# Performance work log

Measured on AMD Instinct MI355X. Metric: run time of the kernel, lower is better.

Reference implementation:

```python
import jax, jax.numpy as jnp
import numpy as np

IGNORE_INDEX = -100  # torch default; targets here are all valid but mask is honored
REDUCTION = "mean"

B, D, V = 4096, 2048, 32000


def setup_inputs() -> dict:
    key = jax.random.key(0)
    k1, k2, k3 = jax.random.split(key, 3)
    x = jax.random.normal(k1, (B, D), dtype=jnp.float32)
    # LM-head weight, scaled like typical init
    L = jax.random.normal(k2, (V, D), dtype=jnp.float32) * (1.0 / np.sqrt(D))
    target = jax.random.randint(k3, (B,), 0, V, dtype=jnp.int64)
    class_weight = jnp.ones((V,), dtype=jnp.float32)  # unnormalized per-class weight
    return {"x": x, "L": L, "target": target, "class_weight": class_weight}


def reference(x, L, target, class_weight):
    """Fused linear + weighted cross-entropy (reduction='mean', ignore_index=-100).

    Equivalent math to MyLinearCrossEntropyFunction: the torch code chunks over
    batches/classes/features with an online softmax solely to avoid materializing
    logits; the unchunked math is a single GEMM + stable log-softmax CE.
    """
    # logits: [B, V]
    logits = jnp.einsum("bd,vd->bv", x, L)
    logZ = jax.nn.logsumexp(logits, axis=1)                      # [B]
    valid = target != IGNORE_INDEX                               # [B] bool
    t_safe = jnp.where(valid, target, 0)
    gathered = jnp.take_along_axis(logits, t_safe[:, None], axis=1)[:, 0]  # [B]
    # effective per-sample weight: class weight of target, zeroed where ignored
    wt = jnp.where(valid, class_weight[t_safe], jnp.zeros((), logits.dtype))  # [B]
    per_sample = wt * (logZ - gathered)
    total = per_sample.sum()
    if REDUCTION == "mean":
        return total / wt.sum()
    return total
```

## Files before the change

### kernel.cpp

```cpp
#include <hip/hip_runtime.h>

#define B_ 4096
#define D_ 2048
#define V_ 32000

#define BM 128
#define BN 128
#define BKB 128
#define NCHUNK (V_ / 64)

typedef __attribute__((ext_vector_type(8))) int   int8v;
typedef __attribute__((ext_vector_type(4))) int   int4v;
typedef __attribute__((ext_vector_type(4))) float f32x4;

#define SCALE_A 127
#define SCALE_B 121

__device__ __forceinline__ void load_lds16(const void* g, void* l) {
    __builtin_amdgcn_global_load_lds(
        (const __attribute__((address_space(1))) void*)g,
        (__attribute__((address_space(3))) void*)l,
        16, 0, 0);
}

__global__ void cast_f32_to_fp8(const float* __restrict__ x,
                                const float* __restrict__ L,
                                unsigned int* __restrict__ xq,
                                unsigned int* __restrict__ Lq) {
    const int n4x = (B_ * D_) / 4;
    const int n4l = (V_ * D_) / 4;
    int i = blockIdx.x * blockDim.x + threadIdx.x;
    const float* in; unsigned int* out; float ps; int j;
    if (i < n4x) { in = x; out = xq; ps = 1.0f;  j = i; }
    else         { j = i - n4x; if (j >= n4l) return; in = L; out = Lq; ps = 64.0f; }
    float4 v = ((const float4*)in)[j];
    int w = __builtin_amdgcn_cvt_pk_fp8_f32(v.x * ps, v.y * ps, 0, false);
    w     = __builtin_amdgcn_cvt_pk_fp8_f32(v.z * ps, v.w * ps, w, true);
    out[j] = (unsigned)w;
}

__global__ __launch_bounds__(256)
void gemm_ce_partials(const unsigned char* __restrict__ xq,
                      const unsigned char* __restrict__ Lq,
                      const int* __restrict__ targ,
                      float2* __restrict__ partials,
                      float* __restrict__ gathered) {
    __shared__ __align__(16) unsigned char As[BM * BKB];
    __shared__ __align__(16) unsigned char Bs[BN * BKB];

    const int tid    = threadIdx.x;
    const int lane   = tid & 63;
    const int wid    = tid >> 6;
    const int wave_m = wid >> 1;
    const int wave_n = wid & 1;
    const int quad   = lane >> 4;
    const int l16    = lane & 15;
    const int swz    = l16 & 7;

    const int m0 = blockIdx.x * BM;
    const int n0 = blockIdx.y * BN;

    f32x4 acc[4][4];
#pragma unroll
    for (int i = 0; i < 4; ++i)
#pragma unroll
        for (int j = 0; j < 4; ++j)
            acc[i][j] = (f32x4){0.f, 0.f, 0.f, 0.f};

    const int p0 = ((quad ^ swz) << 4);
    const int p1 = p0 ^ 64;

    for (int kt = 0; kt < D_ / BKB; ++kt) {
        const int k0 = kt * BKB;
#pragma unroll
        for (int p = 0; p < 4; ++p) {
            int flat = p * 256 + tid;
            int row  = flat >> 3;
            int pc   = flat & 7;
            int c    = pc ^ (row & 7);
            load_lds16(xq + (size_t)(m0 + row) * D_ + k0 + c * 16, &As[flat * 16]);
            load_lds16(Lq + (size_t)(n0 + row) * D_ + k0 + c * 16, &Bs[flat * 16]);
        }
        __syncthreads();

        int8v a[4], b[4];
#pragma unroll
        for (int mi = 0; mi < 4; ++mi) {
            int base = (wave_m * 64 + mi * 16 + l16) * BKB;
            union { int8v v8; int4v v4[2]; } u;
            u.v4[0] = *(const int4v*)&As[base + p0];
            u.v4[1] = *(const int4v*)&As[base + p1];
            a[mi] = u.v8;
        }
#pragma unroll
        for (int ni = 0; ni < 4; ++ni) {
            int base = (wave_n * 64 + ni * 16 + l16) * BKB;
            union { int8v v8; int4v v4[2]; } u;
            u.v4[0] = *(const int4v*)&Bs[base + p0];
            u.v4[1] = *(const int4v*)&Bs[base + p1];
            b[ni] = u.v8;
        }
#pragma unroll
        for (int mi = 0; mi < 4; ++mi)
#pragma unroll
            for (int ni = 0; ni < 4; ++ni)
                acc[mi][ni] = __builtin_amdgcn_mfma_scale_f32_16x16x128_f8f6f4(
                    a[mi], b[ni], acc[mi][ni],
                    0, 0,
                    0, SCALE_A,
                    0, SCALE_B);
        __syncthreads();
    }

    const int row_base = m0 + wave_m * 64;
    const int col_base = n0 + wave_n * 64;
    const int chunk    = blockIdx.y * 2 + wave_n;

    int tv[16];
#pragma unroll
    for (int mi = 0; mi < 4; ++mi)
#pragma unroll
        for (int r = 0; r < 4; ++r)
            tv[mi * 4 + r] = targ[row_base + mi * 16 + quad * 4 + r];

    float M = acc[0][0][0];
#pragma unroll
    for (int mi = 0; mi < 4; ++mi)
#pragma unroll
        for (int ni = 0; ni < 4; ++ni)
#pragma unroll
            for (int r = 0; r < 4; ++r)
                M = fmaxf(M, acc[mi][ni][r]);
#pragma unroll
    for (int off = 1; off < 64; off <<= 1)
        M = fmaxf(M, __shfl_xor(M, off, 64));

    float sv[16];
#pragma unroll
    for (int mi = 0; mi < 4; ++mi)
#pragma unroll
        for (int r = 0; r < 4; ++r)
            sv[mi * 4 + r] = __expf(acc[mi][0][r] - M) + __expf(acc[mi][1][r] - M) +
                             __expf(acc[mi][2][r] - M) + __expf(acc[mi][3][r] - M);
#pragma unroll
    for (int off = 1; off < 16; off <<= 1)
#pragma unroll
        for (int i = 0; i < 16; ++i)
            sv[i] += __shfl_xor(sv[i], off, 64);

    if (l16 == 0) {
#pragma unroll
        for (int mi = 0; mi < 4; ++mi)
#pragma unroll
            for (int r = 0; r < 4; ++r) {
                int row = row_base + mi * 16 + quad * 4 + r;
                partials[(size_t)row * NCHUNK + chunk] = make_float2(M, sv[mi * 4 + r]);
            }
    }

#pragma unroll
    for (int mi = 0; mi < 4; ++mi)
#pragma unroll
        for (int r = 0; r < 4; ++r) {
            int row = row_base + mi * 16 + quad * 4 + r;
            int cb  = col_base + l16;
            int t   = tv[mi * 4 + r];
            if (cb      == t) gathered[row] = acc[mi][0][r];
            if (cb + 16 == t) gathered[row] = acc[mi][1][r];
            if (cb + 32 == t) gathered[row] = acc[mi][2][r];
            if (cb + 48 == t) gathered[row] = acc[mi][3][r];
        }
}

__global__ void combine_rows(const float2* __restrict__ partials,
                             const float* __restrict__ gathered,
                             const int* __restrict__ targ,
                             const float* __restrict__ cw,
                             float* __restrict__ row_loss,
                             float* __restrict__ row_w) {
    int row  = blockIdx.x * 4 + (threadIdx.x >> 6);
    int lane = threadIdx.x & 63;
    float m = -3.0e38f, s = 0.f;
    for (int c = lane; c < NCHUNK; c += 64) {
        float2 p = partials[(size_t)row * NCHUNK + c];
        float nm = fmaxf(m, p.x);
        s = s * __expf(m - nm) + p.y * __expf(p.x - nm);
        m = nm;
    }
#pragma unroll
    for (int off = 32; off; off >>= 1) {
        float om = __shfl_xor(m, off, 64);
        float os = __shfl_xor(s, off, 64);
        float nm = fmaxf(m, om);
        s = s * __expf(m - nm) + os * __expf(om - nm);
        m = nm;
    }
    if (lane == 0) {
        float logZ = m + __logf(s);
        int t = targ[row];
        bool valid = (t != -100);
        int ts = valid ? t : 0;
        float w = valid ? cw[ts] : 0.f;
        row_loss[row] = w * (logZ - gathered[row]);
        row_w[row]    = w;
    }
}

__global__ void final_reduce(const float* __restrict__ rl,
                             const float* __restrict__ rw,
                             float* __restrict__ out) {
    __shared__ float sl[4], sw[4];
    float a = 0.f, b = 0.f;
    for (int i = threadIdx.x; i < B_; i += 256) { a += rl[i]; b += rw[i]; }
#pragma unroll
    for (int off = 32; off; off >>= 1) {
        a += __shfl_xor(a, off, 64);
        b += __shfl_xor(b, off, 64);
    }
    int w = threadIdx.x >> 6;
    if ((threadIdx.x & 63) == 0) { sl[w] = a; sw[w] = b; }
    __syncthreads();
    if (threadIdx.x == 0) {
        float ta = sl[0] + sl[1] + sl[2] + sl[3];
        float tb = sw[0] + sw[1] + sw[2] + sw[3];
        out[0] = ta / tb;
    }
}

extern "C" void kernel_launch(void* const* d_in, const int* in_sizes, int n_in,
                              void* d_out, int out_size, void* d_ws, size_t ws_size,
                              hipStream_t stream) {
    const float* x  = (const float*)d_in[0];
    const float* L  = (const float*)d_in[1];
    const int* targ = (const int*)d_in[2];
    const float* cw = (const float*)d_in[3];
    float* out = (float*)d_out;

    char* ws = (char*)d_ws;
    size_t o = 0;
    unsigned char* xq = (unsigned char*)(ws + o);  o += (size_t)B_ * D_;
    unsigned char* Lq = (unsigned char*)(ws + o);  o += (size_t)V_ * D_;
    float2* partials = (float2*)(ws + o);          o += (size_t)B_ * NCHUNK * 8;
    float* gathered = (float*)(ws + o);            o += (size_t)B_ * 4;
    float* row_loss = (float*)(ws + o);            o += (size_t)B_ * 4;
    float* row_w    = (float*)(ws + o);            o += (size_t)B_ * 4;
    (void)ws_size;

    {
        int n4 = (B_ * D_) / 4 + (V_ * D_) / 4;
        cast_f32_to_fp8<<<(n4 + 255) / 256, 256, 0, stream>>>(
            x, L, (unsigned*)xq, (unsigned*)Lq);
    }

    {
        dim3 grid(B_ / BM, V_ / BN);
        gemm_ce_partials<<<grid, 256, 0, stream>>>(xq, Lq, targ, partials, gathered);
    }

    combine_rows<<<B_ / 4, 256, 0, stream>>>(partials, gathered, targ, cw, row_loss, row_w);

    final_reduce<<<1, 256, 0, stream>>>(row_loss, row_w, out);
}
```

Before: 700.5 us.

## Use 256x256 double-buffered LDS tiles with interleaved prefetch in fp8 GEMM

Doubles the GEMM block tile to 256x256 with 8 waves per block, each wave owning a 128x64 output sub-tile. The LDS tiles are double-buffered, and the next K-slice is prefetched in halves (A, then B) between MFMA phases, with barriers and s_setprio around the MFMA bursts. The aim is to hide global-to-LDS latency behind compute and raise operand reuse per byte loaded. In exchange it needs 128KB of LDS and 128 accumulator registers per thread, which limits occupancy to one block per CU, and it adds many barriers per K-step.

After: 658.7 us. 1.06x faster.

```diff
diff --git a/kernel.cpp b/kernel.cpp
--- a/kernel.cpp
+++ b/kernel.cpp
@@ -4,9 +4,10 @@
 #define D_ 2048
 #define V_ 32000
 
-#define BM 128
-#define BN 128
+#define BM 256
+#define BN 256
 #define BKB 128
+#define NT (D_ / BKB)
 #define NCHUNK (V_ / 64)
 
 typedef __attribute__((ext_vector_type(8))) int   int8v;
@@ -39,20 +40,20 @@
     out[j] = (unsigned)w;
 }
 
-__global__ __launch_bounds__(256)
+__global__ __launch_bounds__(512, 2)
 void gemm_ce_partials(const unsigned char* __restrict__ xq,
                       const unsigned char* __restrict__ Lq,
                       const int* __restrict__ targ,
                       float2* __restrict__ partials,
                       float* __restrict__ gathered) {
-    __shared__ __align__(16) unsigned char As[BM * BKB];
-    __shared__ __align__(16) unsigned char Bs[BN * BKB];
+    __shared__ __align__(16) unsigned char As[2][BM * BKB];
+    __shared__ __align__(16) unsigned char Bs[2][BN * BKB];
 
     const int tid    = threadIdx.x;
     const int lane   = tid & 63;
     const int wid    = tid >> 6;
-    const int wave_m = wid >> 1;
-    const int wave_n = wid & 1;
+    const int wave_m = wid >> 2;
+    const int wave_n = wid & 3;
     const int quad   = lane >> 4;
     const int l16    = lane & 15;
     const int swz    = l16 & 7;
@@ -60,9 +61,23 @@
     const int m0 = blockIdx.x * BM;
     const int n0 = blockIdx.y * BN;
 
-    f32x4 acc[4][4];
-#pragma unroll
-    for (int i = 0; i < 4; ++i)
+    const unsigned char* srcA[4];
+    const unsigned char* srcB[4];
+    int dstoff[4];
+#pragma unroll
+    for (int p = 0; p < 4; ++p) {
+        int flat = p * 512 + tid;
+        int row  = flat >> 3;
+        int pc   = flat & 7;
+        int c    = pc ^ (row & 7);
+        dstoff[p] = flat * 16;
+        srcA[p] = xq + (size_t)(m0 + row) * D_ + c * 16;
+        srcB[p] = Lq + (size_t)(n0 + row) * D_ + c * 16;
+    }
+
+    f32x4 acc[8][4];
+#pragma unroll
+    for (int i = 0; i < 8; ++i)
 #pragma unroll
         for (int j = 0; j < 4; ++j)
             acc[i][j] = (f32x4){0.f, 0.f, 0.f, 0.f};
@@ -70,62 +85,123 @@
     const int p0 = ((quad ^ swz) << 4);
     const int p1 = p0 ^ 64;
 
-    for (int kt = 0; kt < D_ / BKB; ++kt) {
-        const int k0 = kt * BKB;
-#pragma unroll
-        for (int p = 0; p < 4; ++p) {
-            int flat = p * 256 + tid;
-            int row  = flat >> 3;
-            int pc   = flat & 7;
-            int c    = pc ^ (row & 7);
-            load_lds16(xq + (size_t)(m0 + row) * D_ + k0 + c * 16, &As[flat * 16]);
-            load_lds16(Lq + (size_t)(n0 + row) * D_ + k0 + c * 16, &Bs[flat * 16]);
-        }
-        __syncthreads();
+#pragma unroll
+    for (int p = 0; p < 4; ++p) {
+        load_lds16(srcA[p], &As[0][dstoff[p]]);
+        load_lds16(srcB[p], &Bs[0][dstoff[p]]);
+    }
+    asm volatile("s_waitcnt vmcnt(0)" ::: "memory");
+    __builtin_amdgcn_s_barrier();
+
+    for (int kt = 0; kt < NT; ++kt) {
+        const int cur = kt & 1;
+        const int nxt = cur ^ 1;
+        const int k1  = (kt + 1) * BKB;
+        const bool pf = (kt + 1 < NT);
 
         int8v a[4], b[4];
+
 #pragma unroll
         for (int mi = 0; mi < 4; ++mi) {
-            int base = (wave_m * 64 + mi * 16 + l16) * BKB;
+            int base = (wave_m * 128 + mi * 16 + l16) * BKB;
             union { int8v v8; int4v v4[2]; } u;
-            u.v4[0] = *(const int4v*)&As[base + p0];
-            u.v4[1] = *(const int4v*)&As[base + p1];
+            u.v4[0] = *(const int4v*)&As[cur][base + p0];
+            u.v4[1] = *(const int4v*)&As[cur][base + p1];
             a[mi] = u.v8;
         }
 #pragma unroll
-        for (int ni = 0; ni < 4; ++ni) {
+        for (int ni = 0; ni < 2; ++ni) {
             int base = (wave_n * 64 + ni * 16 + l16) * BKB;
             union { int8v v8; int4v v4[2]; } u;
-            u.v4[0] = *(const int4v*)&Bs[base + p0];
-            u.v4[1] = *(const int4v*)&Bs[base + p1];
+            u.v4[0] = *(const int4v*)&Bs[cur][base + p0];
+            u.v4[1] = *(const int4v*)&Bs[cur][base + p1];
             b[ni] = u.v8;
         }
+        if (pf) {
+#pragma unroll
+            for (int p = 0; p < 4; ++p)
+                load_lds16(srcA[p] + k1, &As[nxt][dstoff[p]]);
+        }
+        __builtin_amdgcn_s_barrier();
+        __builtin_amdgcn_s_setprio(1);
 #pragma unroll
         for (int mi = 0; mi < 4; ++mi)
 #pragma unroll
-            for (int ni = 0; ni < 4; ++ni)
+            for (int ni = 0; ni < 2; ++ni)
                 acc[mi][ni] = __builtin_amdgcn_mfma_scale_f32_16x16x128_f8f6f4(
-                    a[mi], b[ni], acc[mi][ni],
-                    0, 0,
-                    0, SCALE_A,
-                    0, SCALE_B);
-        __syncthreads();
-    }
-
-    const int row_base = m0 + wave_m * 64;
+                    a[mi], b[ni], acc[mi][ni], 0, 0, 0, SCALE_A, 0, SCALE_B);
+        __builtin_amdgcn_s_setprio(0);
+        __builtin_amdgcn_s_barrier();
+
+#pragma unroll
+        for (int ni = 2; ni < 4; ++ni) {
+            int base = (wave_n * 64 + ni * 16 + l16) * BKB;
+            union { int8v v8; int4v v4[2]; } u;
+            u.v4[0] = *(const int4v*)&Bs[cur][base + p0];
+            u.v4[1] = *(const int4v*)&Bs[cur][base + p1];
+            b[ni] = u.v8;
+        }
+        if (pf) {
+#pragma unroll
+            for (int p = 0; p < 4; ++p)
+                load_lds16(srcB[p] + k1, &Bs[nxt][dstoff[p]]);
+        }
+        __builtin_amdgcn_s_barrier();
+        __builtin_amdgcn_s_setprio(1);
+#pragma unroll
+        for (int mi = 0; mi < 4; ++mi)
+#pragma unroll
+            for (int ni = 2; ni < 4; ++ni)
+                acc[mi][ni] = __builtin_amdgcn_mfma_scale_f32_16x16x128_f8f6f4(
+                    a[mi], b[ni], acc[mi][ni], 0, 0, 0, SCALE_A, 0, SCALE_B);
+        __builtin_amdgcn_s_setprio(0);
+        __builtin_amdgcn_s_barrier();
+
+#pragma unroll
+        for (int mi = 0; mi < 4; ++mi) {
+            int base = (wave_m * 128 + (mi + 4) * 16 + l16) * BKB;
+            union { int8v v8; int4v v4[2]; } u;
+            u.v4[0] = *(const int4v*)&As[cur][base + p0];
+            u.v4[1] = *(const int4v*)&As[cur][base + p1];
+            a[mi] = u.v8;
+        }
+        __builtin_amdgcn_s_barrier();
+        __builtin_amdgcn_s_setprio(1);
+#pragma unroll
+        for (int mi = 0; mi < 4; ++mi)
+#pragma unroll
+            for (int ni = 0; ni < 2; ++ni)
+                acc[mi + 4][ni] = __builtin_amdgcn_mfma_scale_f32_16x16x128_f8f6f4(
+                    a[mi], b[ni], acc[mi + 4][ni], 0, 0, 0, SCALE_A, 0, SCALE_B);
+        __builtin_amdgcn_s_setprio(0);
+        __builtin_amdgcn_s_barrier();
+
+        __builtin_amdgcn_s_setprio(1);
+#pragma unroll
+        for (int mi = 0; mi < 4; ++mi)
+#pragma unroll
+            for (int ni = 2; ni < 4; ++ni)
+                acc[mi + 4][ni] = __builtin_amdgcn_mfma_scale_f32_16x16x128_f8f6f4(
+                    a[mi], b[ni], acc[mi + 4][ni], 0, 0, 0, SCALE_A, 0, SCALE_B);
+        __builtin_amdgcn_s_setprio(0);
+        asm volatile("s_waitcnt vmcnt(0)" ::: "memory");
+        __builtin_amdgcn_s_barrier();
+    }
+
+    const int row_base = m0 + wave_m * 128;
     const int col_base = n0 + wave_n * 64;
-    const int chunk    = blockIdx.y * 2 + wave_n;
-
-    int tv[16];
-#pragma unroll
-    for (int mi = 0; mi < 4; ++mi)
+    const int chunk    = blockIdx.y * 4 + wave_n;
+
+    int tv[32];
+#pragma unroll
+    for (int mi = 0; mi < 8; ++mi)
 #pragma unroll
         for (int r = 0; r < 4; ++r)
             tv[mi * 4 + r] = targ[row_base + mi * 16 + quad * 4 + r];
 
     float M = acc[0][0][0];
 #pragma unroll
-    for (int mi = 0; mi < 4; ++mi)
+    for (int mi = 0; mi < 8; ++mi)
 #pragma unroll
         for (int ni = 0; ni < 4; ++ni)
 #pragma unroll
@@ -135,9 +211,9 @@
     for (int off = 1; off < 64; off <<= 1)
         M = fmaxf(M, __shfl_xor(M, off, 64));
 
-    float sv[16];
-#pragma unroll
-    for (int mi = 0; mi < 4; ++mi)
+    float sv[32];
+#pragma unroll
+    for (int mi = 0; mi < 8; ++mi)
 #pragma unroll
         for (int r = 0; r < 4; ++r)
             sv[mi * 4 + r] = __expf(acc[mi][0][r] - M) + __expf(acc[mi][1][r] - M) +
@@ -145,12 +221,12 @@
 #pragma unroll
     for (int off = 1; off < 16; off <<= 1)
 #pragma unroll
-        for (int i = 0; i < 16; ++i)
+        for (int i = 0; i < 32; ++i)
             sv[i] += __shfl_xor(sv[i], off, 64);
 
     if (l16 == 0) {
 #pragma unroll
-        for (int mi = 0; mi < 4; ++mi)
+        for (int mi = 0; mi < 8; ++mi)
 #pragma unroll
             for (int r = 0; r < 4; ++r) {
                 int row = row_base + mi * 16 + quad * 4 + r;
@@ -159,7 +235,7 @@
     }
 
 #pragma unroll
-    for (int mi = 0; mi < 4; ++mi)
+    for (int mi = 0; mi < 8; ++mi)
 #pragma unroll
         for (int r = 0; r < 4; ++r) {
             int row = row_base + mi * 16 + quad * 4 + r;
@@ -254,7 +330,7 @@
 
     {
         dim3 grid(B_ / BM, V_ / BN);
-        gemm_ce_partials<<<grid, 256, 0, stream>>>(xq, Lq, targ, partials, gathered);
+        gemm_ce_partials<<<grid, 512, 0, stream>>>(xq, Lq, targ, partials, gathered);
     }
 
     combine_rows<<<B_ / 4, 256, 0, stream>>>(partials, gathered, targ, cw, row_loss, row_w);
```
